# Kernel optimization log

Hardware: AMD Instinct MI355X
Metric: run time of the kernel (lower is better)

Reference implementation:

```python
import jax, jax.numpy as jnp
import numpy as np

B, C_IN, H, W = 8, 64, 256, 256
C_OUT, K, N_KERNELS = 128, 3, 8
PAD = K // 2


def setup_inputs() -> dict:
    key = jax.random.key(0)
    k1, k2, k3, k4 = jax.random.split(key, 4)
    x = jax.random.normal(k1, (B, C_IN, H, W), dtype=jnp.float32)
    kernel_bank = jax.random.normal(k2, (N_KERNELS, C_OUT, C_IN, K, K), dtype=jnp.float32)
    # nn.Linear(in_channels, num_kernels): weight (N, C_IN), bias (N,)
    lim = 1.0 / np.sqrt(C_IN)
    attn_w = jax.random.uniform(k3, (N_KERNELS, C_IN), minval=-lim, maxval=lim, dtype=jnp.float32)
    attn_b = jax.random.uniform(k4, (N_KERNELS,), minval=-lim, maxval=lim, dtype=jnp.float32)
    return {"x": x, "kernel_bank": kernel_bank, "attn_w": attn_w, "attn_b": attn_b}


def _per_sample_conv(xi, wi):
    # xi: (C_IN, H, W), wi: (C_OUT, C_IN, K, K)
    out = jax.lax.conv_general_dilated(
        xi[None], wi, window_strides=(1, 1), padding=[(PAD, PAD), (PAD, PAD)],
        dimension_numbers=("NCHW", "OIHW", "NCHW"))
    return out[0]


def reference(x, kernel_bank, attn_w, attn_b):
    pooled = jnp.mean(x, axis=(2, 3))                      # (B, C_IN)
    logits = pooled @ attn_w.T + attn_b                     # (B, N)
    attn = jax.nn.softmax(logits, axis=1)                   # (B, N)
    # Fused kernel mix: avoid (B, N, O, I, K, K) intermediate
    mixed = jnp.einsum("bn,noihw->boihw", attn, kernel_bank)  # (B, O, I, K, K)
    return jax.vmap(_per_sample_conv)(x, mixed)             # (B, O, H, W)
```

## Files before the change

kernel.cpp:

```cpp
#include <hip/hip_runtime.h>
#include <hip/hip_bf16.h>

#define B_     8
#define C_IN   64
#define C_OUT  128
#define HW     256
#define NK     8
#define KS     3

typedef __attribute__((ext_vector_type(8))) short bf16x8;
typedef __attribute__((ext_vector_type(4))) float f32x4;
typedef __attribute__((ext_vector_type(4))) unsigned int u32x4;

__device__ inline unsigned short f2bf(float f) {
    union { float f; unsigned int u; } a; a.f = f;
    unsigned int u = a.u;
    u += 0x7fffu + ((u >> 16) & 1u);
    return (unsigned short)(u >> 16);
}
__device__ inline float bf2f(unsigned short u) {
    union { float f; unsigned int u; } a; a.u = ((unsigned int)u) << 16; return a.f;
}

#define XT_PLANE  (258 * 64)

__global__ __launch_bounds__(256) void prepass_kernel(const float* __restrict__ x,
                                                      unsigned short* __restrict__ xT,
                                                      float* __restrict__ poolpart) {
    const int hp = blockIdx.x;
    const int b  = blockIdx.y;
    const int t  = threadIdx.x;
    unsigned short* plane = xT + ((size_t)b * 258 + hp) * XT_PLANE;

    if (hp == 0 || hp == 257) {
        f32x4 z = {0.f, 0.f, 0.f, 0.f};
        for (int ofs = t * 16; ofs < XT_PLANE * 2; ofs += 256 * 16)
            *(f32x4*)((char*)plane + ofs) = z;
        return;
    }
    const int h = hp - 1;

    __shared__ unsigned short tile[256 * 66];
    __shared__ float psum[4][64];

    const float* xp = x + ((size_t)b * C_IN * HW + h) * HW + t;
    unsigned int pk[32];
    #pragma unroll
    for (int ci = 0; ci < 32; ci++) {
        float v0 = xp[(size_t)(2 * ci) * (HW * HW)];
        float v1 = xp[(size_t)(2 * ci + 1) * (HW * HW)];
        unsigned int p = (unsigned int)f2bf(v0) | ((unsigned int)f2bf(v1) << 16);
        pk[ci] = p;
        *(unsigned int*)&tile[t * 66 + 2 * ci] = p;
    }

    unsigned short* rowp = plane + (size_t)(t + 1) * 64;
    const int sw = (t + 1) & 7;
    #pragma unroll
    for (int j = 0; j < 8; j++) {
        u32x4 v; v[0] = pk[4*j]; v[1] = pk[4*j+1]; v[2] = pk[4*j+2]; v[3] = pk[4*j+3];
        *(u32x4*)(rowp + (size_t)((j ^ sw) * 8)) = v;
    }
    if (t < 2) {
        unsigned short* zr = plane + (size_t)(t ? 257 : 0) * 64;
        f32x4 z = {0.f, 0.f, 0.f, 0.f};
        #pragma unroll
        for (int j = 0; j < 8; j++) *(f32x4*)((char*)zr + j * 16) = z;
    }

    __syncthreads();
    const int c = t & 63, part = t >> 6;
    float s = 0.f;
    #pragma unroll 8
    for (int i = 0; i < 64; i++)
        s += bf2f(tile[(part * 64 + i) * 66 + c]);
    psum[part][c] = s;
    __syncthreads();
    if (t < 64)
        poolpart[((size_t)b * 258 + hp) * 64 + t] =
            (psum[0][t] + psum[1][t]) + (psum[2][t] + psum[3][t]);
}

__global__ __launch_bounds__(256) void attn_kernel(const float* __restrict__ poolpart,
                                                   const float* __restrict__ attn_w,
                                                   const float* __restrict__ attn_b,
                                                   float* __restrict__ attn) {
    const int b = blockIdx.x;
    const int t = threadIdx.x;
    const int c = t & 63, part = t >> 6;
    __shared__ float psum[4][64];
    __shared__ float pooled[64];
    __shared__ float logits[NK];

    float s = 0.f;
    const float* pp = poolpart + ((size_t)b * 258) * 64 + c;
    for (int hp = part * 64 + 1; hp <= part * 64 + 64; hp++)
        s += pp[(size_t)hp * 64];
    psum[part][c] = s;
    __syncthreads();
    if (t < 64)
        pooled[t] = ((psum[0][t] + psum[1][t]) + (psum[2][t] + psum[3][t]))
                    * (1.0f / (HW * HW));
    __syncthreads();
    if (t < NK) {
        float l = attn_b[t];
        #pragma unroll 8
        for (int cc = 0; cc < C_IN; cc++) l += pooled[cc] * attn_w[t * C_IN + cc];
        logits[t] = l;
    }
    __syncthreads();
    if (t < NK) {
        float m = -1e30f;
        #pragma unroll
        for (int j = 0; j < NK; j++) m = fmaxf(m, logits[j]);
        float denom = 0.f;
        #pragma unroll
        for (int j = 0; j < NK; j++) denom += expf(logits[j] - m);
        attn[b * NK + t] = expf(logits[t] - m) / denom;
    }
}

__global__ __launch_bounds__(256) void mix_kernel(const float* __restrict__ bank,
                                                  const float* __restrict__ attn,
                                                  unsigned short* __restrict__ Wt2) {
    const int PER_B = C_OUT * C_IN * KS * KS;
    int idx = blockIdx.x * 256 + threadIdx.x;
    int b = idx / PER_B;
    int r = idx % PER_B;
    float s = 0.f;
    #pragma unroll
    for (int n = 0; n < NK; n++) s += attn[b * NK + n] * bank[(size_t)n * PER_B + r];
    int kw = r % 3;
    int t1 = r / 3;
    int kh = t1 % 3;
    int t2 = t1 / 3;
    int i = t2 & 63;
    int o = t2 >> 6;
    size_t off = (((size_t)((b * 3 + kh) * 3 + kw) * 2 + (i >> 5)) * 128 + o) * 32 + (i & 31);
    Wt2[off] = f2bf(s);
}

__global__ __launch_bounds__(256, 2) void conv_mfma5(const unsigned short* __restrict__ xT,
                                                     const short* __restrict__ Wt2,
                                                     float* __restrict__ out) {
    const int flat = blockIdx.y * HW + blockIdx.x;
    const int work = (flat & 7) * (HW * B_ / 8) + (flat >> 3);
    const int b = work >> 8;
    const int h = work & 255;

    const int t    = threadIdx.x;
    const int lane = t & 63;
    const int wid  = t >> 6;
    const int l15  = lane & 15;
    const int quad = lane >> 4;
    const int wn   = wid * 64;
    const int r0   = wn + l15;

    const short* Ab = Wt2 + (size_t)b * (9 * 2 * 4096) + l15 * 32 + quad * 8;
    const unsigned short* xb = xT + (size_t)b * 258 * XT_PLANE;

    f32x4 acc[8][4];
    #pragma unroll
    for (int m = 0; m < 8; m++)
        #pragma unroll
        for (int nt = 0; nt < 4; nt++)
            acc[m][nt] = (f32x4){0.f, 0.f, 0.f, 0.f};

    #pragma unroll
    for (int kh = 0; kh < 3; kh++) {
        const unsigned short* hpb = xb + (size_t)(h + kh) * XT_PLANE;
        #pragma unroll
        for (int kw = 0; kw < 3; kw++) {
            const int rr = r0 + kw;
            const unsigned short* rowb = hpb + rr * 64;
            const int rx = rr & 7;
            #pragma unroll
            for (int ic = 0; ic < 2; ic++) {
                const int s = (kh * 3 + kw) * 2 + ic;
                bf16x8 Bv[4];
                #pragma unroll
                for (int nt = 0; nt < 4; nt++)
                    Bv[nt] = *(const bf16x8*)(rowb + nt * 1024
                                              + ((((ic << 2) + quad) ^ rx) << 3));
                bf16x8 Av[8];
                #pragma unroll
                for (int m = 0; m < 8; m++)
                    Av[m] = *(const bf16x8*)(Ab + s * 4096 + m * 512);
                #pragma unroll
                for (int m = 0; m < 8; m++) {
                    #pragma unroll
                    for (int nt = 0; nt < 4; nt++)
                        acc[m][nt] = __builtin_amdgcn_mfma_f32_16x16x32_bf16(
                            Av[m], Bv[nt], acc[m][nt], 0, 0, 0);
                }
            }
        }
    }

    #pragma unroll
    for (int m = 0; m < 8; m++) {
        const int o = m * 16 + quad * 4;
        #pragma unroll
        for (int nt = 0; nt < 4; nt++) {
            const int w = wn + nt * 16 + l15;
            float* op = out + (((size_t)(b * C_OUT + o) * HW + h) * HW + w);
            #pragma unroll
            for (int r = 0; r < 4; r++) op[(size_t)r * HW * HW] = acc[m][nt][r];
        }
    }
}

__global__ __launch_bounds__(256) void pool_kernel(const float* __restrict__ x,
                                                   float* __restrict__ pooled) {
    const int plane = blockIdx.x;
    const float4* p = (const float4*)(x + (size_t)plane * HW * HW);
    float s = 0.f;
    for (int idx = threadIdx.x; idx < (HW * HW) / 4; idx += 256) {
        float4 v = p[idx];
        s += v.x + v.y + v.z + v.w;
    }
    #pragma unroll
    for (int off = 32; off > 0; off >>= 1) s += __shfl_down(s, off, 64);
    __shared__ float ls[4];
    const int lane = threadIdx.x & 63, wv = threadIdx.x >> 6;
    if (lane == 0) ls[wv] = s;
    __syncthreads();
    if (threadIdx.x == 0) {
        float t = ls[0] + ls[1] + ls[2] + ls[3];
        pooled[plane] = t * (1.0f / (HW * HW));
    }
}

__global__ void attn_legacy(const float* __restrict__ pooled,
                            const float* __restrict__ attn_w,
                            const float* __restrict__ attn_b,
                            float* __restrict__ attn) {
    const int t = threadIdx.x;
    const int b = t >> 3, n = t & 7;
    float s = attn_b[n];
    #pragma unroll 8
    for (int c = 0; c < C_IN; c++) s += pooled[b * C_IN + c] * attn_w[n * C_IN + c];
    __shared__ float logits[B_ * NK];
    logits[t] = s;
    __syncthreads();
    float m = -1e30f;
    #pragma unroll
    for (int j = 0; j < NK; j++) m = fmaxf(m, logits[b * NK + j]);
    float denom = 0.f;
    #pragma unroll
    for (int j = 0; j < NK; j++) denom += expf(logits[b * NK + j] - m);
    attn[t] = expf(s - m) / denom;
}

__global__ __launch_bounds__(256) void conv_mfma(const float* __restrict__ x,
                                                 const short* __restrict__ Wt2,
                                                 float* __restrict__ out) {
    const int w0 = blockIdx.x * 128;
    const int h  = blockIdx.y;
    const int b  = blockIdx.z;
    const int t    = threadIdx.x;
    const int lane = t & 63;
    const int wid  = t >> 6;
    const int wm   = (wid & 1) * 64;
    const int wn   = (wid >> 1) * 64;
    const int l15  = lane & 15;
    const int quad = lane >> 4;
    __shared__ short sxs[130 * 72];
    f32x4 acc[4][4];
    #pragma unroll
    for (int mt = 0; mt < 4; mt++)
        #pragma unroll
        for (int nt = 0; nt < 4; nt++)
            acc[mt][nt] = (f32x4){0.f, 0.f, 0.f, 0.f};
    for (int kh = 0; kh < 3; kh++) {
        __syncthreads();
        const int hr = h + kh - 1;
        const bool rv = (hr >= 0) && (hr < HW);
        {
            const int wl = t & 127;
            const int w  = w0 + wl - 1;
            const bool wvalid = rv && (w >= 0) && (w < HW);
            #pragma unroll
            for (int it = 0; it < 16; it++) {
                const int ip = it * 2 + (t >> 7);
                float v0 = 0.f, v1 = 0.f;
                if (wvalid) {
                    const float* px = x + (((size_t)(b * C_IN + 2 * ip) * HW + hr) * HW + w);
                    v0 = px[0];
                    v1 = px[HW * HW];
                }
                ushort2 u;
                u.x = f2bf(v0);
                u.y = f2bf(v1);
                *(ushort2*)&sxs[wl * 72 + 2 * ip] = u;
            }
            if (t < 128) {
                const int i2  = t >> 1;
                const int wl2 = 128 + (t & 1);
                const int w2  = w0 + wl2 - 1;
                unsigned short uv = 0;
                if (rv && w2 < HW)
                    uv = f2bf(x[((size_t)(b * C_IN + i2) * HW + hr) * HW + w2]);
                ((unsigned short*)sxs)[wl2 * 72 + i2] = uv;
            }
        }
        __syncthreads();
        const short* wbase = Wt2 + (size_t)((b * 3 + kh) * 3) * 2 * 4096;
        #pragma unroll
        for (int kw = 0; kw < 3; kw++) {
            #pragma unroll
            for (int ic = 0; ic < 2; ic++) {
                const short* Ap = wbase + (size_t)(kw * 2 + ic) * 4096
                                + (wm + l15) * 32 + quad * 8;
                bf16x8 a0 = *(const bf16x8*)(Ap);
                bf16x8 a1 = *(const bf16x8*)(Ap + 512);
                bf16x8 a2 = *(const bf16x8*)(Ap + 1024);
                bf16x8 a3 = *(const bf16x8*)(Ap + 1536);
                const short* Bp = sxs + (wn + l15 + kw) * 72 + ic * 32 + quad * 8;
                bf16x8 b0 = *(const bf16x8*)(Bp);
                bf16x8 b1 = *(const bf16x8*)(Bp + 16 * 72);
                bf16x8 b2 = *(const bf16x8*)(Bp + 32 * 72);
                bf16x8 b3 = *(const bf16x8*)(Bp + 48 * 72);
                acc[0][0] = __builtin_amdgcn_mfma_f32_16x16x32_bf16(a0, b0, acc[0][0], 0, 0, 0);
                acc[0][1] = __builtin_amdgcn_mfma_f32_16x16x32_bf16(a0, b1, acc[0][1], 0, 0, 0);
                acc[0][2] = __builtin_amdgcn_mfma_f32_16x16x32_bf16(a0, b2, acc[0][2], 0, 0, 0);
                acc[0][3] = __builtin_amdgcn_mfma_f32_16x16x32_bf16(a0, b3, acc[0][3], 0, 0, 0);
                acc[1][0] = __builtin_amdgcn_mfma_f32_16x16x32_bf16(a1, b0, acc[1][0], 0, 0, 0);
                acc[1][1] = __builtin_amdgcn_mfma_f32_16x16x32_bf16(a1, b1, acc[1][1], 0, 0, 0);
                acc[1][2] = __builtin_amdgcn_mfma_f32_16x16x32_bf16(a1, b2, acc[1][2], 0, 0, 0);
                acc[1][3] = __builtin_amdgcn_mfma_f32_16x16x32_bf16(a1, b3, acc[1][3], 0, 0, 0);
                acc[2][0] = __builtin_amdgcn_mfma_f32_16x16x32_bf16(a2, b0, acc[2][0], 0, 0, 0);
                acc[2][1] = __builtin_amdgcn_mfma_f32_16x16x32_bf16(a2, b1, acc[2][1], 0, 0, 0);
                acc[2][2] = __builtin_amdgcn_mfma_f32_16x16x32_bf16(a2, b2, acc[2][2], 0, 0, 0);
                acc[2][3] = __builtin_amdgcn_mfma_f32_16x16x32_bf16(a2, b3, acc[2][3], 0, 0, 0);
                acc[3][0] = __builtin_amdgcn_mfma_f32_16x16x32_bf16(a3, b0, acc[3][0], 0, 0, 0);
                acc[3][1] = __builtin_amdgcn_mfma_f32_16x16x32_bf16(a3, b1, acc[3][1], 0, 0, 0);
                acc[3][2] = __builtin_amdgcn_mfma_f32_16x16x32_bf16(a3, b2, acc[3][2], 0, 0, 0);
                acc[3][3] = __builtin_amdgcn_mfma_f32_16x16x32_bf16(a3, b3, acc[3][3], 0, 0, 0);
            }
        }
    }
    #pragma unroll
    for (int mt = 0; mt < 4; mt++) {
        const int o = wm + mt * 16 + quad * 4;
        #pragma unroll
        for (int nt = 0; nt < 4; nt++) {
            const int w = w0 + wn + nt * 16 + l15;
            float* op = out + (((size_t)(b * C_OUT + o) * HW + h) * HW + w);
            #pragma unroll
            for (int r = 0; r < 4; r++) op[(size_t)r * HW * HW] = acc[mt][nt][r];
        }
    }
}

extern "C" void kernel_launch(void* const* d_in, const int* in_sizes, int n_in,
                              void* d_out, int out_size, void* d_ws, size_t ws_size,
                              hipStream_t stream) {
    const float* x      = (const float*)d_in[0];
    const float* bank   = (const float*)d_in[1];
    const float* attn_w = (const float*)d_in[2];
    const float* attn_b = (const float*)d_in[3];
    float* out = (float*)d_out;

    const size_t XT_BYTES  = (size_t)B_ * 258 * XT_PLANE * sizeof(short);
    const size_t WT2_BYTES = (size_t)B_ * C_OUT * C_IN * KS * KS * sizeof(short);
    const size_t PP_BYTES  = (size_t)B_ * 258 * 64 * sizeof(float);
    const size_t NEED = XT_BYTES + WT2_BYTES + PP_BYTES + (size_t)(B_ * NK) * 4 + 256;

    if (ws_size >= NEED) {
        unsigned short* xT  = (unsigned short*)d_ws;
        unsigned short* Wt2 = (unsigned short*)((char*)d_ws + XT_BYTES);
        float* poolpart = (float*)((char*)d_ws + XT_BYTES + WT2_BYTES);
        float* attn     = poolpart + (size_t)B_ * 258 * 64;

        prepass_kernel<<<dim3(258, B_), 256, 0, stream>>>(x, xT, poolpart);
        attn_kernel<<<B_, 256, 0, stream>>>(poolpart, attn_w, attn_b, attn);
        mix_kernel<<<(B_ * C_OUT * C_IN * KS * KS) / 256, 256, 0, stream>>>(bank, attn, Wt2);
        conv_mfma5<<<dim3(HW, B_), 256, 0, stream>>>(xT, (const short*)Wt2, out);
    } else {
        unsigned short* Wt2 = (unsigned short*)d_ws;
        float* pooled = (float*)((char*)d_ws + 589824 * sizeof(short));
        float* attn   = pooled + B_ * C_IN;
        pool_kernel<<<B_ * C_IN, 256, 0, stream>>>(x, pooled);
        attn_legacy<<<1, 64, 0, stream>>>(pooled, attn_w, attn_b, attn);
        mix_kernel<<<(B_ * C_OUT * C_IN * KS * KS) / 256, 256, 0, stream>>>(bank, attn, Wt2);
        conv_mfma<<<dim3(2, HW, B_), 256, 0, stream>>>(x, (const short*)Wt2, out);
    }
}
```

Before: 495.5 us.

## Retile conv into 64-wide column blocks with LDS-staged input rows

The conv kernel now tiles each output row into four 64-column blocks. Each block's four waves split as a 2x2 grid over output channels and columns. The three input rows the tile needs are copied into shared memory with global_load_lds, so activation fragments are reused from LDS rather than reloaded from global memory. The accumulator tile per wave shrinks from 8x4 to 4x2, which lowers register pressure and allows launch bounds of 4 blocks per CU. The trade-off is that weight fragments are reloaded four times more often across blocks, and every block now has a barrier.

New measurement: 523.3 us. 1.06x slower.

```diff
diff --git a/kernel.cpp b/kernel.cpp
--- a/kernel.cpp
+++ b/kernel.cpp
@@ -140,72 +140,87 @@
     Wt2[off] = f2bf(s);
 }
 
-__global__ __launch_bounds__(256, 2) void conv_mfma5(const unsigned short* __restrict__ xT,
+__global__ __launch_bounds__(256, 4) void conv_mfma7(const unsigned short* __restrict__ xT,
                                                      const short* __restrict__ Wt2,
                                                      float* __restrict__ out) {
-    const int flat = blockIdx.y * HW + blockIdx.x;
-    const int work = (flat & 7) * (HW * B_ / 8) + (flat >> 3);
-    const int b = work >> 8;
-    const int h = work & 255;
+    const int b  = blockIdx.x;
+    const int w0 = blockIdx.y * 64;
+    const int h  = blockIdx.z;
 
     const int t    = threadIdx.x;
     const int lane = t & 63;
     const int wid  = t >> 6;
+    const int wm   = (wid >> 1) * 64;
+    const int wnn  = (wid & 1) * 32;
     const int l15  = lane & 15;
     const int quad = lane >> 4;
-    const int wn   = wid * 64;
-    const int r0   = wn + l15;
-
-    const short* Ab = Wt2 + (size_t)b * (9 * 2 * 4096) + l15 * 32 + quad * 8;
-    const unsigned short* xb = xT + (size_t)b * 258 * XT_PLANE;
-
-    f32x4 acc[8][4];
-    #pragma unroll
-    for (int m = 0; m < 8; m++)
-        #pragma unroll
-        for (int nt = 0; nt < 4; nt++)
-            acc[m][nt] = (f32x4){0.f, 0.f, 0.f, 0.f};
+
+    __shared__ short sxs[3 * 4224];
 
     #pragma unroll
     for (int kh = 0; kh < 3; kh++) {
-        const unsigned short* hpb = xb + (size_t)(h + kh) * XT_PLANE;
+        const char* src = (const char*)(xT + (((size_t)b * 258 + (size_t)(h + kh)) * 258
+                                              + (size_t)w0) * 64);
+        char* dst = (char*)sxs + kh * 8448;
+        const int wo = wid * 2048;
+        __builtin_amdgcn_global_load_lds((const __attribute__((address_space(1))) void*)(src + wo + lane * 16),
+                                         (__attribute__((address_space(3))) void*)(dst + wo), 16, 0, 0);
+        __builtin_amdgcn_global_load_lds((const __attribute__((address_space(1))) void*)(src + wo + 1024 + lane * 16),
+                                         (__attribute__((address_space(3))) void*)(dst + wo + 1024), 16, 0, 0);
+        if (wid == 3)
+            __builtin_amdgcn_global_load_lds((const __attribute__((address_space(1))) void*)(src + 8192 + lane * 4),
+                                             (__attribute__((address_space(3))) void*)(dst + 8192), 4, 0, 0);
+    }
+    __syncthreads();
+
+    const short* wt_b = Wt2 + (size_t)b * (9 * 2 * 4096);
+
+    f32x4 acc[4][2];
+    #pragma unroll
+    for (int mt = 0; mt < 4; mt++)
+        #pragma unroll
+        for (int nt = 0; nt < 2; nt++)
+            acc[mt][nt] = (f32x4){0.f, 0.f, 0.f, 0.f};
+
+    #pragma unroll
+    for (int kh = 0; kh < 3; kh++) {
         #pragma unroll
         for (int kw = 0; kw < 3; kw++) {
-            const int rr = r0 + kw;
-            const unsigned short* rowb = hpb + rr * 64;
-            const int rx = rr & 7;
+            const int row = wnn + l15 + kw;
+            const short* rowp = sxs + kh * 4224 + row * 64;
+            const int rx = row & 7;
             #pragma unroll
             for (int ic = 0; ic < 2; ic++) {
                 const int s = (kh * 3 + kw) * 2 + ic;
-                bf16x8 Bv[4];
-                #pragma unroll
-                for (int nt = 0; nt < 4; nt++)
-                    Bv[nt] = *(const bf16x8*)(rowb + nt * 1024
-                                              + ((((ic << 2) + quad) ^ rx) << 3));
-                bf16x8 Av[8];
-                #pragma unroll
-                for (int m = 0; m < 8; m++)
-                    Av[m] = *(const bf16x8*)(Ab + s * 4096 + m * 512);
-                #pragma unroll
-                for (int m = 0; m < 8; m++) {
-                    #pragma unroll
-                    for (int nt = 0; nt < 4; nt++)
-                        acc[m][nt] = __builtin_amdgcn_mfma_f32_16x16x32_bf16(
-                            Av[m], Bv[nt], acc[m][nt], 0, 0, 0);
-                }
+                const short* Ap = wt_b + s * 4096 + (wm + l15) * 32 + quad * 8;
+                bf16x8 a0 = *(const bf16x8*)(Ap);
+                bf16x8 a1 = *(const bf16x8*)(Ap + 512);
+                bf16x8 a2 = *(const bf16x8*)(Ap + 1024);
+                bf16x8 a3 = *(const bf16x8*)(Ap + 1536);
+                const short* Bp = rowp + ((((ic << 2) + quad) ^ rx) << 3);
+                bf16x8 b0 = *(const bf16x8*)(Bp);
+                bf16x8 b1 = *(const bf16x8*)(Bp + 1024);
+                acc[0][0] = __builtin_amdgcn_mfma_f32_16x16x32_bf16(a0, b0, acc[0][0], 0, 0, 0);
+                acc[0][1] = __builtin_amdgcn_mfma_f32_16x16x32_bf16(a0, b1, acc[0][1], 0, 0, 0);
+                acc[1][0] = __builtin_amdgcn_mfma_f32_16x16x32_bf16(a1, b0, acc[1][0], 0, 0, 0);
+                acc[1][1] = __builtin_amdgcn_mfma_f32_16x16x32_bf16(a1, b1, acc[1][1], 0, 0, 0);
+                acc[2][0] = __builtin_amdgcn_mfma_f32_16x16x32_bf16(a2, b0, acc[2][0], 0, 0, 0);
+                acc[2][1] = __builtin_amdgcn_mfma_f32_16x16x32_bf16(a2, b1, acc[2][1], 0, 0, 0);
+                acc[3][0] = __builtin_amdgcn_mfma_f32_16x16x32_bf16(a3, b0, acc[3][0], 0, 0, 0);
+                acc[3][1] = __builtin_amdgcn_mfma_f32_16x16x32_bf16(a3, b1, acc[3][1], 0, 0, 0);
             }
         }
     }
 
     #pragma unroll
-    for (int m = 0; m < 8; m++) {
-        const int o = m * 16 + quad * 4;
-        #pragma unroll
-        for (int nt = 0; nt < 4; nt++) {
-            const int w = wn + nt * 16 + l15;
+    for (int mt = 0; mt < 4; mt++) {
+        const int o = wm + mt * 16 + quad * 4;
+        #pragma unroll
+        for (int nt = 0; nt < 2; nt++) {
+            const int w = w0 + wnn + nt * 16 + l15;
             float* op = out + (((size_t)(b * C_OUT + o) * HW + h) * HW + w);
             #pragma unroll
-            for (int r = 0; r < 4; r++) op[(size_t)r * HW * HW] = acc[m][nt][r];
+            for (int r = 0; r < 4; r++) op[(size_t)r * HW * HW] = acc[mt][nt][r];
         }
     }
 }
@@ -376,7 +391,7 @@
         prepass_kernel<<<dim3(258, B_), 256, 0, stream>>>(x, xT, poolpart);
         attn_kernel<<<B_, 256, 0, stream>>>(poolpart, attn_w, attn_b, attn);
         mix_kernel<<<(B_ * C_OUT * C_IN * KS * KS) / 256, 256, 0, stream>>>(bank, attn, Wt2);
-        conv_mfma5<<<dim3(HW, B_), 256, 0, stream>>>(xT, (const short*)Wt2, out);
+        conv_mfma7<<<dim3(B_, 4, HW), 256, 0, stream>>>(xT, (const short*)Wt2, out);
     } else {
         unsigned short* Wt2 = (unsigned short*)d_ws;
         float* pooled = (float*)((char*)d_ws + 589824 * sizeof(short));
```
